# Performance work log

Hardware: AMD Instinct MI355X
Metric: run time of the kernel (lower is better)

## Reference

```python
import jax, jax.numpy as jnp
import numpy as np

GAMMA = 0.5

def _rbf_gram(a, b):
    # exp(-gamma * ||a - b||^2), computed via the expanded quadratic form.
    # a: [N, d], b: [M, d] -> [N, M]
    a2 = jnp.sum(a * a, axis=-1)                      # [N]
    b2 = jnp.sum(b * b, axis=-1)                      # [M]
    sq = a2[:, None] + b2[None, :] - 2.0 * (a @ b.T)  # [N, M]
    return jnp.exp(-GAMMA * jnp.maximum(sq, 0.0))


def setup_inputs() -> dict:
    key = jax.random.key(0)
    kx, kp = jax.random.split(key)
    x = jax.random.normal(kx, (32768, 16), dtype=jnp.float32)
    particles = jax.random.normal(kp, (8192, 16), dtype=jnp.float32)
    return {"x": x, "particles": particles}


def reference(x, particles):
    n_p = particles.shape[0]
    # p=None, norm=True -> px = ones(N_x) / N_x
    px = jnp.ones(x.shape[0], dtype=x.dtype) / x.shape[0]
    t1 = jnp.mean(_rbf_gram(particles, particles))           # mean over [N_p, N_p]
    t2 = 2.0 * jnp.sum(px @ _rbf_gram(x, particles)) / n_p   # weighted row-sum of [N_x, N_p]
    return t1 - t2
```

## Files before the change

### kernel.cpp

```cpp
#include <hip/hip_runtime.h>
#include <hip/hip_bf16.h>

#define THREADS 256
#define DIM 16

typedef __attribute__((ext_vector_type(8))) short bf16x8;
typedef __attribute__((ext_vector_type(16))) float f32x16;
typedef __attribute__((ext_vector_type(2))) float f32x2;

__device__ __forceinline__ float rawexp2(float a) { return __builtin_amdgcn_exp2f(a); }

__global__ __launch_bounds__(THREADS) void prep_kernel(
    const float* __restrict__ x, int nx,
    const float* __restrict__ p, int np,
    short* __restrict__ xbs, float* __restrict__ xn,
    short* __restrict__ pbs, short* __restrict__ pb,
    float* __restrict__ pn, float* __restrict__ pfp)
{
    const float L2E  = 1.44269504088896340736f;
    const float HL2E = 0.72134752044448170368f;
    int i = blockIdx.x * THREADS + threadIdx.x;
    const float* src; short* ds; short* dp; float* dn; float* df;
    if (i < nx) {
        src = x + (size_t)i * DIM; ds = xbs + (size_t)i * DIM;
        dp = nullptr; dn = xn + i; df = nullptr;
    } else if (i < nx + np) {
        int j = i - nx;
        src = p + (size_t)j * DIM; ds = pbs + (size_t)j * DIM;
        dp = pb + (size_t)j * DIM; dn = pn + j; df = pfp + j;
    } else {
        return;
    }

    float nrm = 0.f;
    bf16x8 plo, phi, slo, shi;
#pragma unroll
    for (int k = 0; k < DIM; ++k) {
        unsigned u = __float_as_uint(src[k]);
        unsigned short r = (unsigned short)((u + 0x7FFFu + ((u >> 16) & 1u)) >> 16);
        float fr = __uint_as_float((unsigned)r << 16);
        nrm = fmaf(fr, fr, nrm);
        unsigned us = __float_as_uint(L2E * fr);
        unsigned short rs = (unsigned short)((us + 0x7FFFu + ((us >> 16) & 1u)) >> 16);
        if (k < 8) { plo[k] = (short)r; slo[k] = (short)rs; }
        else       { phi[k - 8] = (short)r; shi[k - 8] = (short)rs; }
    }
    *(bf16x8*)ds = slo; *((bf16x8*)ds + 1) = shi;
    if (dp) { *(bf16x8*)dp = plo; *((bf16x8*)dp + 1) = phi; }
    float ns = -HL2E * nrm;
    *dn = ns;
    if (df) *df = rawexp2(ns);
}

__device__ __forceinline__ void consume_tile(const f32x16& d, float f, f32x2& acc)
{
    f32x2 pf2 = {f, f};
#pragma unroll
    for (int r = 0; r < 8; ++r) {
        f32x2 e = { rawexp2(d[2 * r]), rawexp2(d[2 * r + 1]) };
        acc = e * pf2 + acc;
    }
}

__device__ __forceinline__ float gram_phase(
    const short* __restrict__ rowsb, const float* __restrict__ rown,
    const short* __restrict__ colsb, const float* __restrict__ colpf,
    int row0, int ct0, int ntiles, int l31, int half)
{
    bf16x8 afrag = *(const bf16x8*)(rowsb + (size_t)(row0 + l31) * DIM + half * 8);

    f32x16 cseed;
#pragma unroll
    for (int r = 0; r < 16; ++r) {
        int rrow = (r & 3) + 8 * (r >> 2) + 4 * half;
        cseed[r] = rown[row0 + rrow];
    }

    const short* bptr = colsb + ((size_t)ct0 * 32 + l31) * DIM + half * 8;
    const float* fptr = colpf + ct0 * 32 + l31;
    const size_t bstride = (size_t)32 * DIM;

    bf16x8 b0 = *(const bf16x8*)bptr;
    bf16x8 b1 = *(const bf16x8*)(bptr + bstride);
    float  f0 = fptr[0];
    float  f1 = fptr[32];

    f32x16 d0 = __builtin_amdgcn_mfma_f32_32x32x16_bf16(afrag, b0, cseed, 0, 0, 0);
    f32x16 d1 = __builtin_amdgcn_mfma_f32_32x32x16_bf16(afrag, b1, cseed, 0, 0, 0);

    f32x2 acc = {0.f, 0.f};

    for (int t = 0; t + 2 < ntiles; t += 2) {
        bf16x8 bn0 = *(const bf16x8*)(bptr + (size_t)(t + 2) * bstride);
        float  fn0 = fptr[(t + 2) * 32];
        bf16x8 bn1 = *(const bf16x8*)(bptr + (size_t)(t + 3) * bstride);
        float  fn1 = fptr[(t + 3) * 32];

        consume_tile(d0, f0, acc);
        d0 = __builtin_amdgcn_mfma_f32_32x32x16_bf16(afrag, bn0, cseed, 0, 0, 0);
        consume_tile(d1, f1, acc);
        d1 = __builtin_amdgcn_mfma_f32_32x32x16_bf16(afrag, bn1, cseed, 0, 0, 0);

        f0 = fn0; f1 = fn1;
    }
    consume_tile(d0, f0, acc);
    consume_tile(d1, f1, acc);
    return acc.x + acc.y;
}

__global__ __launch_bounds__(THREADS) void gram_fused_kernel(
    const short* __restrict__ xbs, const float* __restrict__ xn,
    const short* __restrict__ pbs, const short* __restrict__ pb,
    const float* __restrict__ pn, const float* __restrict__ pfp,
    int nrt_p, int n1,
    int nrt_x, int n2,
    double sc1, double sc2,
    double* __restrict__ partials)
{
    const int lane = threadIdx.x & 63;
    const int wv   = threadIdx.x >> 6;
    const int l31  = lane & 31;
    const int half = lane >> 5;
    const int w    = blockIdx.x * (THREADS / 64) + wv;

    const int rt1 = w & (nrt_p - 1);
    const int c10 = (w / nrt_p) * n1;
    float acc1 = gram_phase(pbs, pn, pb, pfp, rt1 * 32, c10, n1, l31, half);

    const int rt2 = w & (nrt_x - 1);
    const int c20 = (w / nrt_x) * n2;
    float acc2 = gram_phase(xbs, xn, pb, pfp, rt2 * 32, c20, n2, l31, half);

    double v = (double)acc1 * sc1 - (double)acc2 * sc2;
#pragma unroll
    for (int off = 32; off > 0; off >>= 1) v += __shfl_down(v, off);

    __shared__ double sred[THREADS / 64];
    if (lane == 0) sred[wv] = v;
    __syncthreads();
    if (threadIdx.x == 0) {
        double tot = 0.0;
#pragma unroll
        for (int q = 0; q < THREADS / 64; ++q) tot += sred[q];
        partials[blockIdx.x] = tot;
    }
}

__global__ __launch_bounds__(THREADS) void finalize_kernel(
    const double* __restrict__ partials, int n, float* __restrict__ out)
{
    double v = 0.0;
    for (int i = threadIdx.x; i < n; i += THREADS) v += partials[i];
#pragma unroll
    for (int off = 32; off > 0; off >>= 1) v += __shfl_down(v, off);

    __shared__ double sred[THREADS / 64];
    const int lane = threadIdx.x & 63;
    const int wid = threadIdx.x >> 6;
    if (lane == 0) sred[wid] = v;
    __syncthreads();
    if (threadIdx.x == 0) {
        double tot = 0.0;
#pragma unroll
        for (int q = 0; q < THREADS / 64; ++q) tot += sred[q];
        out[0] = (float)tot;
    }
}

extern "C" void kernel_launch(void* const* d_in, const int* in_sizes, int n_in,
                              void* d_out, int out_size, void* d_ws, size_t ws_size,
                              hipStream_t stream) {
    const float* x = (const float*)d_in[0];
    const float* particles = (const float*)d_in[1];
    float* out = (float*)d_out;

    const int NX = in_sizes[0] / DIM;
    const int NP = in_sizes[1] / DIM;

    const int nrt_x = NX / 32;
    const int nrt_p = NP / 32;

    const int NBLOCKS = 1024;
    const int WAVES = NBLOCKS * (THREADS / 64);
    const int n1 = (nrt_p * nrt_p) / WAVES;
    const int n2 = (nrt_x * nrt_p) / WAVES;

    char* ws = (char*)d_ws;
    double* partials = (double*)ws;
    float*  xn  = (float*)(ws + 16384);
    float*  pn  = (float*)(ws + 147456);
    float*  pfp = (float*)(ws + 180224);
    short*  xbs = (short*)(ws + 212992);
    short*  pbs = (short*)(ws + 1261568);
    short*  pb  = (short*)(ws + 1523712);

    const int nprep = (NX + NP + THREADS - 1) / THREADS;
    prep_kernel<<<nprep, THREADS, 0, stream>>>(x, NX, particles, NP,
                                               xbs, xn, pbs, pb, pn, pfp);

    gram_fused_kernel<<<NBLOCKS, THREADS, 0, stream>>>(
        xbs, xn, pbs, pb, pn, pfp,
        nrt_p, n1, nrt_x, n2,
        1.0 / ((double)NP * (double)NP),
        2.0 / ((double)NX * (double)NP),
        partials);

    finalize_kernel<<<1, THREADS, 0, stream>>>(partials, NBLOCKS, out);
}
```

Baseline: 50.72 us.

## Process two row tiles per wave to reuse column fragments, fully unroll

Each wave now handles a 64-row pair of tiles against a column strip, so every loaded column fragment and weight feeds two MFMAs instead of one, halving column-operand loads per output. The tile counts are fixed as template parameters (8 and 32) and the loop is fully unrolled with a two-deep prefetch ring. Work decomposition constants are hardcoded for the given problem size (128/512 row pairs), removing generality and raising register pressure.

```diff
diff --git a/kernel.cpp b/kernel.cpp
--- a/kernel.cpp
+++ b/kernel.cpp
@@ -62,58 +62,55 @@
     }
 }
 
-__device__ __forceinline__ float gram_phase(
+template<int NT>
+__device__ __forceinline__ void pair_phase(
     const short* __restrict__ rowsb, const float* __restrict__ rown,
     const short* __restrict__ colsb, const float* __restrict__ colpf,
-    int row0, int ct0, int ntiles, int l31, int half)
-{
-    bf16x8 afrag = *(const bf16x8*)(rowsb + (size_t)(row0 + l31) * DIM + half * 8);
-
-    f32x16 cseed;
+    int row0, int ct0, int l31, int half,
+    float& outA, float& outB)
+{
+    bf16x8 a0 = *(const bf16x8*)(rowsb + (size_t)(row0 + l31) * DIM + half * 8);
+    bf16x8 a1 = *(const bf16x8*)(rowsb + (size_t)(row0 + 32 + l31) * DIM + half * 8);
+
+    f32x16 c0, c1;
 #pragma unroll
     for (int r = 0; r < 16; ++r) {
         int rrow = (r & 3) + 8 * (r >> 2) + 4 * half;
-        cseed[r] = rown[row0 + rrow];
+        c0[r] = rown[row0 + rrow];
+        c1[r] = rown[row0 + 32 + rrow];
     }
 
     const short* bptr = colsb + ((size_t)ct0 * 32 + l31) * DIM + half * 8;
     const float* fptr = colpf + ct0 * 32 + l31;
     const size_t bstride = (size_t)32 * DIM;
 
-    bf16x8 b0 = *(const bf16x8*)bptr;
-    bf16x8 b1 = *(const bf16x8*)(bptr + bstride);
-    float  f0 = fptr[0];
-    float  f1 = fptr[32];
-
-    f32x16 d0 = __builtin_amdgcn_mfma_f32_32x32x16_bf16(afrag, b0, cseed, 0, 0, 0);
-    f32x16 d1 = __builtin_amdgcn_mfma_f32_32x32x16_bf16(afrag, b1, cseed, 0, 0, 0);
-
-    f32x2 acc = {0.f, 0.f};
-
-    for (int t = 0; t + 2 < ntiles; t += 2) {
-        bf16x8 bn0 = *(const bf16x8*)(bptr + (size_t)(t + 2) * bstride);
-        float  fn0 = fptr[(t + 2) * 32];
-        bf16x8 bn1 = *(const bf16x8*)(bptr + (size_t)(t + 3) * bstride);
-        float  fn1 = fptr[(t + 3) * 32];
-
-        consume_tile(d0, f0, acc);
-        d0 = __builtin_amdgcn_mfma_f32_32x32x16_bf16(afrag, bn0, cseed, 0, 0, 0);
-        consume_tile(d1, f1, acc);
-        d1 = __builtin_amdgcn_mfma_f32_32x32x16_bf16(afrag, bn1, cseed, 0, 0, 0);
-
-        f0 = fn0; f1 = fn1;
-    }
-    consume_tile(d0, f0, acc);
-    consume_tile(d1, f1, acc);
-    return acc.x + acc.y;
+    bf16x8 bq[2]; float fq[2];
+    bq[0] = *(const bf16x8*)bptr;            fq[0] = fptr[0];
+    bq[1] = *(const bf16x8*)(bptr + bstride); fq[1] = fptr[32];
+
+    f32x2 accA = {0.f, 0.f}, accB = {0.f, 0.f};
+
+#pragma unroll
+    for (int t = 0; t < NT; ++t) {
+        bf16x8 bcur = bq[t & 1];
+        float  pf   = fq[t & 1];
+        if (t + 2 < NT) {
+            bq[t & 1] = *(const bf16x8*)(bptr + (size_t)(t + 2) * bstride);
+            fq[t & 1] = fptr[(t + 2) * 32];
+        }
+        f32x16 d0 = __builtin_amdgcn_mfma_f32_32x32x16_bf16(a0, bcur, c0, 0, 0, 0);
+        f32x16 d1 = __builtin_amdgcn_mfma_f32_32x32x16_bf16(a1, bcur, c1, 0, 0, 0);
+        consume_tile(d0, pf, accA);
+        consume_tile(d1, pf, accB);
+    }
+    outA = accA.x + accA.y;
+    outB = accB.x + accB.y;
 }
 
 __global__ __launch_bounds__(THREADS) void gram_fused_kernel(
     const short* __restrict__ xbs, const float* __restrict__ xn,
     const short* __restrict__ pbs, const short* __restrict__ pb,
     const float* __restrict__ pn, const float* __restrict__ pfp,
-    int nrt_p, int n1,
-    int nrt_x, int n2,
     double sc1, double sc2,
     double* __restrict__ partials)
 {
@@ -123,15 +120,22 @@
     const int half = lane >> 5;
     const int w    = blockIdx.x * (THREADS / 64) + wv;
 
-    const int rt1 = w & (nrt_p - 1);
-    const int c10 = (w / nrt_p) * n1;
-    float acc1 = gram_phase(pbs, pn, pb, pfp, rt1 * 32, c10, n1, l31, half);
-
-    const int rt2 = w & (nrt_x - 1);
-    const int c20 = (w / nrt_x) * n2;
-    float acc2 = gram_phase(xbs, xn, pb, pfp, rt2 * 32, c20, n2, l31, half);
-
-    double v = (double)acc1 * sc1 - (double)acc2 * sc2;
+    float a1s, b1s;
+    {
+        const int rp = w & 127;
+        const int c0 = (w >> 7) * 8;
+        pair_phase<8>(pbs, pn, pb, pfp, rp * 64, c0, l31, half, a1s, b1s);
+    }
+
+    float a2s, b2s;
+    {
+        const int rp = w & 511;
+        const int c0 = (w >> 9) * 32;
+        pair_phase<32>(xbs, xn, pb, pfp, rp * 64, c0, l31, half, a2s, b2s);
+    }
+
+    double v = ((double)a1s + (double)b1s) * sc1
+             - ((double)a2s + (double)b2s) * sc2;
 #pragma unroll
     for (int off = 32; off > 0; off >>= 1) v += __shfl_down(v, off);
 
@@ -177,13 +181,7 @@
     const int NX = in_sizes[0] / DIM;
     const int NP = in_sizes[1] / DIM;
 
-    const int nrt_x = NX / 32;
-    const int nrt_p = NP / 32;
-
     const int NBLOCKS = 1024;
-    const int WAVES = NBLOCKS * (THREADS / 64);
-    const int n1 = (nrt_p * nrt_p) / WAVES;
-    const int n2 = (nrt_x * nrt_p) / WAVES;
 
     char* ws = (char*)d_ws;
     double* partials = (double*)ws;
@@ -200,7 +198,6 @@
 
     gram_fused_kernel<<<NBLOCKS, THREADS, 0, stream>>>(
         xbs, xn, pbs, pb, pn, pfp,
-        nrt_p, n1, nrt_x, n2,
         1.0 / ((double)NP * (double)NP),
         2.0 / ((double)NX * (double)NP),
         partials);
```

Result: slower. 195.6 us (+285.6%).
